# Optimization experiments

Measured on AMD Instinct MI355X. Metric: run time of the kernel, lower is better.

The kernel has to match this reference:

```python
import jax, jax.numpy as jnp
import numpy as np

N = 10000
E = 320000

def gcn_layer(x, W, edge_src, edge_dst, edge_weight):
    # support = x @ W ; out = spmm(adj, support) via edge-list scatter-add
    support = x @ W                                  # [N, H]
    msgs = edge_weight[:, None] * support[edge_src]  # [E, H] gather (irregular)
    return jax.ops.segment_sum(msgs, edge_dst, num_segments=N)

def setup_inputs() -> dict:
    key = jax.random.key(0)
    ks = jax.random.split(key, 7)
    F_in, H1, H2 = 3000, 512, 64
    x = jax.random.normal(ks[0], (N, F_in), dtype=jnp.float32)
    edge_src = jax.random.randint(ks[1], (E,), 0, N)
    edge_dst = jax.random.randint(ks[2], (E,), 0, N)
    edge_weight = jax.random.uniform(ks[3], (E,), dtype=jnp.float32)
    W1 = jax.random.normal(ks[4], (F_in, H1), dtype=jnp.float32) * (1.0 / np.sqrt(F_in))
    W2 = jax.random.normal(ks[5], (H1, H2), dtype=jnp.float32) * (1.0 / np.sqrt(H1))
    W3 = jax.random.normal(ks[6], (H1, H2), dtype=jnp.float32) * (1.0 / np.sqrt(H1))
    return {"x": x, "edge_src": edge_src, "edge_dst": edge_dst,
            "edge_weight": edge_weight, "W1": W1, "W2": W2, "W3": W3}

def reference(x, edge_src, edge_dst, edge_weight, W1, W2, W3):
    # Eval mode: dropout is identity, reparameterize returns mu.
    h1 = jax.nn.relu(gcn_layer(x, W1, edge_src, edge_dst, edge_weight))  # [N, H1]
    mu = gcn_layer(h1, W2, edge_src, edge_dst, edge_weight)              # [N, H2]
    logvar = gcn_layer(h1, W3, edge_src, edge_dst, edge_weight)          # [N, H2]
    z = mu
    pred = z @ z.T  # InnerProductDecoder with act = identity -> [N, N]
    return (pred, mu, logvar)
```

## Files before the change

### kernel.cpp

```cpp
#include <hip/hip_runtime.h>
#include <hip/hip_bf16.h>

#define N_NODES 10000
#define N_EDGES 320000
#define F_IN    3000
#define KP      3008
#define H1      512
#define H2      64
#define CAP     128
#define NT      (KP / 32)

typedef float  f32x4  __attribute__((ext_vector_type(4)));
typedef short  bf16x8 __attribute__((ext_vector_type(8)));
typedef unsigned short us8 __attribute__((ext_vector_type(8)));

__device__ __forceinline__ unsigned short f2b(float f) {
    union { float f; unsigned u; } v; v.f = f;
    unsigned r = v.u + 0x7FFF + ((v.u >> 16) & 1);
    return (unsigned short)(r >> 16);
}
__device__ __forceinline__ float b2f(unsigned short b) {
    union { unsigned u; float f; } v; v.u = ((unsigned)b) << 16;
    return v.f;
}

#define GLOAD_LDS16(gptr, lptr)                                                             \
    __builtin_amdgcn_global_load_lds((const __attribute__((address_space(1))) void*)(gptr), \
                                     (__attribute__((address_space(3))) void*)(lptr),       \
                                     16, 0, 0)

#define NB_BUCKET 1250
#define NB_CONVX  14688
#define NB_CONVW  376

__global__ __launch_bounds__(256) void prep(const int* __restrict__ src,
                                            const int* __restrict__ dst,
                                            const float* __restrict__ w,
                                            const float* __restrict__ x,
                                            const float* __restrict__ W1,
                                            int* __restrict__ cnt,
                                            int* __restrict__ bsrc,
                                            float* __restrict__ bw,
                                            unsigned short* __restrict__ xb,
                                            unsigned short* __restrict__ w1t) {
    __shared__ float tr[64][65];
    const int b = blockIdx.x;
    const int t = threadIdx.x;
    if (b < NB_BUCKET) {
        int e = b * 256 + t;
        if (e >= N_EDGES) return;
        int d = dst[e];
        int slot = atomicAdd(&cnt[d], 1);
        if (slot < CAP) {
            bsrc[d * CAP + slot] = src[e];
            bw[d * CAP + slot]   = w[e];
        }
    } else if (b < NB_BUCKET + NB_CONVX) {
        int idx = (b - NB_BUCKET) * 256 + t;
        int r = idx / (KP / 8);
        int g = idx % (KP / 8);
        if (r >= N_NODES) return;
        us8 v;
        if (g * 8 + 8 <= F_IN) {
            float4 a = *(const float4*)&x[(size_t)r * F_IN + g * 8];
            float4 c = *(const float4*)&x[(size_t)r * F_IN + g * 8 + 4];
            v[0] = f2b(a.x); v[1] = f2b(a.y); v[2] = f2b(a.z); v[3] = f2b(a.w);
            v[4] = f2b(c.x); v[5] = f2b(c.y); v[6] = f2b(c.z); v[7] = f2b(c.w);
        } else {
            #pragma unroll
            for (int j = 0; j < 8; ++j) {
                int k = g * 8 + j;
                v[j] = (k < F_IN) ? f2b(x[(size_t)r * F_IN + k]) : (unsigned short)0;
            }
        }
        *(us8*)&xb[(size_t)r * KP + g * 8] = v;
    } else {
        int bb = b - NB_BUCKET - NB_CONVX;
        int kBase = (bb >> 3) * 64;
        int cBase = (bb & 7) * 64;
        int col = cBase + (t & 63);
        #pragma unroll
        for (int i = 0; i < 16; ++i) {
            int row = kBase + i * 4 + (t >> 6);
            float v = (row < F_IN) ? W1[(size_t)row * H1 + col] : 0.f;
            tr[t & 63][i * 4 + (t >> 6)] = v;
        }
        __syncthreads();
        int c = t >> 2, kq = (t & 3) * 16;
        us8 o0, o1;
        #pragma unroll
        for (int j = 0; j < 8; ++j) { o0[j] = f2b(tr[c][kq + j]); o1[j] = f2b(tr[c][kq + 8 + j]); }
        *(us8*)&w1t[(size_t)(cBase + c) * KP + kBase + kq]     = o0;
        *(us8*)&w1t[(size_t)(cBase + c) * KP + kBase + kq + 8] = o1;
    }
}

__global__ __launch_bounds__(256, 6) void gemm1_mfma(const unsigned short* __restrict__ xb,
                                                     const unsigned short* __restrict__ w1t,
                                                     unsigned short* __restrict__ Cb) {
    __shared__ unsigned short As[2][128 * 32];
    __shared__ unsigned short Bs[2][64 * 32];
    const int f  = blockIdx.x;
    const int k8 = f & 7;
    const int jj = f >> 3;
    const int bx = k8 * 10 + (jj >> 3);
    const int by = jj & 7;
    const int mBase = bx * 128;
    const int nBase = by * 64;

    const int t = threadIdx.x;
    const int wid = t >> 6, lane = t & 63;
    const int wr = (wid >> 1) * 64;
    const int wc = (wid & 1) * 32;
    const int fr = lane & 15;
    const int swz = (((lane >> 4) ^ (fr & 3)) << 3);

    const int srow   = lane >> 2;
    const int schunk = ((lane & 3) ^ (srow & 3)) * 8;
    const int arow0  = min(mBase + wid * 16 + srow, N_NODES - 1);
    const int arow1  = min(mBase + (wid + 4) * 16 + srow, N_NODES - 1);
    const int brow   = nBase + wid * 16 + srow;

    f32x4 acc[4][2] = {};

#define STAGE1(c, k0)                                                              \
    do {                                                                           \
        GLOAD_LDS16(&xb[(size_t)arow0 * KP + (k0) + schunk], &As[c][wid * 512]);   \
        GLOAD_LDS16(&xb[(size_t)arow1 * KP + (k0) + schunk], &As[c][(wid + 4) * 512]); \
        GLOAD_LDS16(&w1t[(size_t)brow * KP + (k0) + schunk], &Bs[c][wid * 512]);   \
    } while (0)

#define COMPUTE1(c)                                                            \
    do {                                                                       \
        bf16x8 af[4], bfv[2];                                                  \
        _Pragma("unroll")                                                      \
        for (int m = 0; m < 4; ++m)                                            \
            af[m] = *(const bf16x8*)&As[c][(wr + m * 16 + fr) * 32 + swz];     \
        _Pragma("unroll")                                                      \
        for (int n = 0; n < 2; ++n)                                            \
            bfv[n] = *(const bf16x8*)&Bs[c][(wc + n * 16 + fr) * 32 + swz];    \
        _Pragma("unroll")                                                      \
        for (int m = 0; m < 4; ++m)                                            \
            _Pragma("unroll")                                                  \
            for (int n = 0; n < 2; ++n)                                        \
                acc[m][n] = __builtin_amdgcn_mfma_f32_16x16x32_bf16(af[m], bfv[n], acc[m][n], 0, 0, 0); \
    } while (0)

    STAGE1(0, 0);
    int cur = 0;
    for (int tt = 0; tt < NT - 1; ++tt) {
        STAGE1(cur ^ 1, (tt + 1) * 32);
        asm volatile("s_waitcnt vmcnt(3)" ::: "memory");
        __builtin_amdgcn_s_barrier();
        __builtin_amdgcn_sched_barrier(0);
        COMPUTE1(cur);
        asm volatile("s_waitcnt lgkmcnt(0)" ::: "memory");
        __builtin_amdgcn_sched_barrier(0);
        __builtin_amdgcn_s_barrier();
        cur ^= 1;
    }
    asm volatile("s_waitcnt vmcnt(0)" ::: "memory");
    __builtin_amdgcn_s_barrier();
    COMPUTE1(cur);

#undef STAGE1
#undef COMPUTE1

    #pragma unroll
    for (int m = 0; m < 4; ++m) {
        int rbase = mBase + wr + m * 16 + (lane >> 4) * 4;
        #pragma unroll
        for (int n = 0; n < 2; ++n) {
            int col = nBase + wc + n * 16 + (lane & 15);
            #pragma unroll
            for (int i = 0; i < 4; ++i) {
                int row = rbase + i;
                if (row < N_NODES)
                    Cb[(size_t)row * H1 + col] = f2b(acc[m][n][i]);
            }
        }
    }
}

__global__ __launch_bounds__(512) void gather_gemm23(const unsigned short* __restrict__ sup,
                                                     const int* __restrict__ cnt,
                                                     const int* __restrict__ bsrc,
                                                     const float* __restrict__ bw,
                                                     const float* __restrict__ W2,
                                                     const float* __restrict__ W3,
                                                     unsigned short* __restrict__ sup2b) {
    __shared__ float hs[16][H1];
    const int t = threadIdx.x;
    const int wid = t >> 6, lane = t & 63;
    const int rBase = blockIdx.x * 16;

    #pragma unroll
    for (int i = 0; i < 2; ++i) {
        const int local = wid * 2 + i;
        const int n = rBase + local;
        const int deg = min(cnt[n], CAP);
        float acc[8] = {};
        for (int e = 0; e < deg; ++e) {
            int   s = bsrc[n * CAP + e];
            float w = bw[n * CAP + e];
            us8 v = *(const us8*)&sup[(size_t)s * H1 + lane * 8];
            #pragma unroll
            for (int j = 0; j < 8; ++j) acc[j] += w * b2f(v[j]);
        }
        *(float4*)&hs[local][lane * 8] =
            make_float4(fmaxf(acc[0], 0.f), fmaxf(acc[1], 0.f), fmaxf(acc[2], 0.f), fmaxf(acc[3], 0.f));
        *(float4*)&hs[local][lane * 8 + 4] =
            make_float4(fmaxf(acc[4], 0.f), fmaxf(acc[5], 0.f), fmaxf(acc[6], 0.f), fmaxf(acc[7], 0.f));
    }
    __syncthreads();

    const int col = t & 127;
    const int rg  = (t >> 7) * 4;
    const float* W = (col < 64) ? (W2 + col) : (W3 + (col - 64));
    float acc2[4] = {};
    for (int k = 0; k < H1; ++k) {
        float wv = W[k * 64];
        #pragma unroll
        for (int i = 0; i < 4; ++i) acc2[i] += wv * hs[rg + i][k];
    }
    #pragma unroll
    for (int i = 0; i < 4; ++i)
        sup2b[(size_t)(rBase + rg + i) * 128 + col] = f2b(acc2[i]);
}

__global__ __launch_bounds__(256) void gather_muvar(const unsigned short* __restrict__ sup2b,
                                                    const int* __restrict__ cnt,
                                                    const int* __restrict__ bsrc,
                                                    const float* __restrict__ bw,
                                                    float* __restrict__ mu,
                                                    float* __restrict__ lv,
                                                    unsigned short* __restrict__ mub) {
    const int n  = blockIdx.x * 16 + (threadIdx.x >> 4);
    const int c8 = (threadIdx.x & 15) * 8;
    const int deg = min(cnt[n], CAP);
    float acc[8] = {};
    for (int e = 0; e < deg; ++e) {
        int   s = bsrc[n * CAP + e];
        float w = bw[n * CAP + e];
        us8 v = *(const us8*)&sup2b[(size_t)s * 128 + c8];
        #pragma unroll
        for (int j = 0; j < 8; ++j) acc[j] += w * b2f(v[j]);
    }
    if (c8 < 64) {
        *(float4*)&mu[(size_t)n * 64 + c8]     = make_float4(acc[0], acc[1], acc[2], acc[3]);
        *(float4*)&mu[(size_t)n * 64 + c8 + 4] = make_float4(acc[4], acc[5], acc[6], acc[7]);
        us8 o;
        #pragma unroll
        for (int j = 0; j < 8; ++j) o[j] = f2b(acc[j]);
        *(us8*)&mub[(size_t)n * 64 + c8] = o;
    } else {
        *(float4*)&lv[(size_t)n * 64 + (c8 - 64)]     = make_float4(acc[0], acc[1], acc[2], acc[3]);
        *(float4*)&lv[(size_t)n * 64 + (c8 - 64) + 4] = make_float4(acc[4], acc[5], acc[6], acc[7]);
    }
}

__global__ __launch_bounds__(256) void pred_mfma(const unsigned short* __restrict__ mub,
                                                 float* __restrict__ pred) {
    __shared__ float st[4][16][68];
    const int t = threadIdx.x, wid = t >> 6, lane = t & 63;
    const int rb = blockIdx.x * 128 + (wid >> 1) * 64;
    const int cb = blockIdx.y * 128 + (wid & 1) * 64;
    const int fr = lane & 15, fk = (lane >> 4) * 8;
    f32x4 acc[4][4] = {};

    #pragma unroll
    for (int ks = 0; ks < 2; ++ks) {
        bf16x8 af[4], bfv[4];
        #pragma unroll
        for (int m = 0; m < 4; ++m) {
            int r = min(rb + m * 16 + fr, N_NODES - 1);
            af[m] = *(const bf16x8*)&mub[(size_t)r * 64 + ks * 32 + fk];
        }
        #pragma unroll
        for (int n = 0; n < 4; ++n) {
            int c = min(cb + n * 16 + fr, N_NODES - 1);
            bfv[n] = *(const bf16x8*)&mub[(size_t)c * 64 + ks * 32 + fk];
        }
        #pragma unroll
        for (int m = 0; m < 4; ++m)
            #pragma unroll
            for (int n = 0; n < 4; ++n)
                acc[m][n] = __builtin_amdgcn_mfma_f32_16x16x32_bf16(af[m], bfv[n], acc[m][n], 0, 0, 0);
    }

    #pragma unroll
    for (int m = 0; m < 4; ++m) {
        #pragma unroll
        for (int n = 0; n < 4; ++n)
            #pragma unroll
            for (int i = 0; i < 4; ++i)
                st[wid][(lane >> 4) * 4 + i][n * 16 + (lane & 15)] = acc[m][n][i];
        int rbase = rb + m * 16;
        #pragma unroll
        for (int it = 0; it < 4; ++it) {
            int row   = it * 4 + (lane >> 4);
            int chunk = lane & 15;
            int grow  = rbase + row;
            int gcol  = cb + chunk * 4;
            if (grow < N_NODES) {
                f32x4 v = *(const f32x4*)&st[wid][row][chunk * 4];
                if (gcol + 3 < N_NODES) {
                    __builtin_nontemporal_store(v, (f32x4*)&pred[(size_t)grow * N_NODES + gcol]);
                } else {
                    #pragma unroll
                    for (int j = 0; j < 4; ++j)
                        if (gcol + j < N_NODES)
                            __builtin_nontemporal_store(v[j], &pred[(size_t)grow * N_NODES + gcol + j]);
                }
            }
        }
    }
}

extern "C" void kernel_launch(void* const* d_in, const int* in_sizes, int n_in,
                              void* d_out, int out_size, void* d_ws, size_t ws_size,
                              hipStream_t stream) {
    const float* x    = (const float*)d_in[0];
    const int*   esrc = (const int*)d_in[1];
    const int*   edst = (const int*)d_in[2];
    const float* ew   = (const float*)d_in[3];
    const float* W1   = (const float*)d_in[4];
    const float* W2   = (const float*)d_in[5];
    const float* W3   = (const float*)d_in[6];

    float* pred = (float*)d_out;
    float* mu   = pred + (size_t)N_NODES * N_NODES;
    float* lv   = mu   + (size_t)N_NODES * H2;

    char* ws = (char*)d_ws;
    unsigned short* sup1b = (unsigned short*)ws; ws += (size_t)N_NODES * H1 * sizeof(short);
    unsigned short* sup2b = (unsigned short*)ws; ws += (size_t)N_NODES * 2 * H2 * sizeof(short);
    int*   cnt      = (int*)ws;   ws += (size_t)N_NODES * sizeof(int);
    int*   bsrc     = (int*)ws;   ws += (size_t)N_NODES * CAP * sizeof(int);
    float* bw       = (float*)ws; ws += (size_t)N_NODES * CAP * sizeof(float);
    unsigned short* xb  = (unsigned short*)ws; ws += (size_t)N_NODES * KP * sizeof(short);
    unsigned short* w1t = (unsigned short*)ws; ws += (size_t)H1 * KP * sizeof(short);
    unsigned short* mub = (unsigned short*)ws; ws += (size_t)N_NODES * H2 * sizeof(short);

    (void)hipMemsetAsync(cnt, 0, N_NODES * sizeof(int), stream);
    prep<<<NB_BUCKET + NB_CONVX + NB_CONVW, 256, 0, stream>>>(esrc, edst, ew, x, W1,
                                                              cnt, bsrc, bw, xb, w1t);
    gemm1_mfma<<<640, 256, 0, stream>>>(xb, w1t, sup1b);
    gather_gemm23<<<N_NODES / 16, 512, 0, stream>>>(sup1b, cnt, bsrc, bw, W2, W3, sup2b);
    gather_muvar<<<N_NODES / 16, 256, 0, stream>>>(sup2b, cnt, bsrc, bw, mu, lv, mub);
    pred_mfma<<<dim3((N_NODES + 127) / 128, (N_NODES + 127) / 128), 256, 0, stream>>>(mub, pred);
}
```

Before: 323.4 us.

## Triple-buffer LDS in gemm1 to prefetch two K-tiles ahead

After: 325.0 us. No clear change (+0.5%).

```diff
diff --git a/kernel.cpp b/kernel.cpp
--- a/kernel.cpp
+++ b/kernel.cpp
@@ -95,11 +95,11 @@
     }
 }
 
-__global__ __launch_bounds__(256, 6) void gemm1_mfma(const unsigned short* __restrict__ xb,
+__global__ __launch_bounds__(256, 4) void gemm1_mfma(const unsigned short* __restrict__ xb,
                                                      const unsigned short* __restrict__ w1t,
                                                      unsigned short* __restrict__ Cb) {
-    __shared__ unsigned short As[2][128 * 32];
-    __shared__ unsigned short Bs[2][64 * 32];
+    __shared__ unsigned short As[3][128 * 32];
+    __shared__ unsigned short Bs[3][64 * 32];
     const int f  = blockIdx.x;
     const int k8 = f & 7;
     const int jj = f >> 3;
@@ -123,22 +123,26 @@
 
     f32x4 acc[4][2] = {};
 
-#define STAGE1(c, k0)                                                              \
-    do {                                                                           \
-        GLOAD_LDS16(&xb[(size_t)arow0 * KP + (k0) + schunk], &As[c][wid * 512]);   \
-        GLOAD_LDS16(&xb[(size_t)arow1 * KP + (k0) + schunk], &As[c][(wid + 4) * 512]); \
-        GLOAD_LDS16(&w1t[(size_t)brow * KP + (k0) + schunk], &Bs[c][wid * 512]);   \
+#define STAGE1(buf, k0)                                                                \
+    do {                                                                               \
+        unsigned short* ab = &As[buf][0];                                              \
+        unsigned short* bb = &Bs[buf][0];                                              \
+        GLOAD_LDS16(&xb[(size_t)arow0 * KP + (k0) + schunk], ab + wid * 512);          \
+        GLOAD_LDS16(&xb[(size_t)arow1 * KP + (k0) + schunk], ab + (wid + 4) * 512);    \
+        GLOAD_LDS16(&w1t[(size_t)brow * KP + (k0) + schunk], bb + wid * 512);          \
     } while (0)
 
-#define COMPUTE1(c)                                                            \
+#define COMPUTE1(buf)                                                          \
     do {                                                                       \
+        const unsigned short* ar = &As[buf][0];                                \
+        const unsigned short* br = &Bs[buf][0];                                \
         bf16x8 af[4], bfv[2];                                                  \
         _Pragma("unroll")                                                      \
         for (int m = 0; m < 4; ++m)                                            \
-            af[m] = *(const bf16x8*)&As[c][(wr + m * 16 + fr) * 32 + swz];     \
+            af[m] = *(const bf16x8*)&ar[(wr + m * 16 + fr) * 32 + swz];        \
         _Pragma("unroll")                                                      \
         for (int n = 0; n < 2; ++n)                                            \
-            bfv[n] = *(const bf16x8*)&Bs[c][(wc + n * 16 + fr) * 32 + swz];    \
+            bfv[n] = *(const bf16x8*)&br[(wc + n * 16 + fr) * 32 + swz];       \
         _Pragma("unroll")                                                      \
         for (int m = 0; m < 4; ++m)                                            \
             _Pragma("unroll")                                                  \
@@ -147,21 +151,29 @@
     } while (0)
 
     STAGE1(0, 0);
-    int cur = 0;
-    for (int tt = 0; tt < NT - 1; ++tt) {
-        STAGE1(cur ^ 1, (tt + 1) * 32);
-        asm volatile("s_waitcnt vmcnt(3)" ::: "memory");
+    STAGE1(1, 32);
+    int cs = 0;
+    int ss = 2;
+    for (int tt = 0; tt < NT - 2; ++tt) {
+        STAGE1(ss, (tt + 2) * 32);
+        asm volatile("s_waitcnt vmcnt(6)" ::: "memory");
         __builtin_amdgcn_s_barrier();
         __builtin_amdgcn_sched_barrier(0);
-        COMPUTE1(cur);
+        COMPUTE1(cs);
         asm volatile("s_waitcnt lgkmcnt(0)" ::: "memory");
         __builtin_amdgcn_sched_barrier(0);
         __builtin_amdgcn_s_barrier();
-        cur ^= 1;
-    }
+        cs = (cs == 2) ? 0 : cs + 1;
+        ss = (ss == 2) ? 0 : ss + 1;
+    }
+    asm volatile("s_waitcnt vmcnt(3)" ::: "memory");
+    __builtin_amdgcn_s_barrier();
+    __builtin_amdgcn_sched_barrier(0);
+    COMPUTE1(cs);
+    cs = (cs == 2) ? 0 : cs + 1;
     asm volatile("s_waitcnt vmcnt(0)" ::: "memory");
     __builtin_amdgcn_s_barrier();
-    COMPUTE1(cur);
+    COMPUTE1(cs);
 
 #undef STAGE1
 #undef COMPUTE1
```
